# Kernel tuning notes

Hardware: AMD Instinct MI355X
Metric: run time of the kernel (lower is better)

Reference implementation:

```python
import jax, jax.numpy as jnp
import numpy as np

B, S, DDENSE, D, V, F, K = 8192, 26, 13, 32, 100000, 8, 7


def setup_inputs() -> dict:
    key = jax.random.key(0)
    ks = jax.random.split(key, 24)
    n = lambda i, shape, s=0.05: (jax.random.normal(ks[i], shape, dtype=jnp.float32) * s)
    return {
        'sparse_inputs': jax.random.randint(ks[0], (B, S), 0, V),
        'dense_inputs': jax.random.normal(ks[1], (B, DDENSE), dtype=jnp.float32),
        'gen_table': n(2, (V, D), 0.1), 'gen_W': n(3, (DDENSE, D)), 'gen_b': jnp.zeros((D,), jnp.float32),
        'cls_table': n(4, (V, D), 0.1), 'cls_W': n(5, (DDENSE, D)), 'cls_b': jnp.zeros((D,), jnp.float32),
        'conv_k0': n(6, (K, 1, 1, F)), 'conv_b0': jnp.zeros((F,), jnp.float32),
        'fc_W0': n(7, (13 * D * F, 3 * D)), 'fc_b0': jnp.zeros((3 * D,), jnp.float32),
        'conv_k1': n(8, (K, 1, F, F)), 'conv_b1': jnp.zeros((F,), jnp.float32),
        'fc_W1': n(9, (6 * D * F, 3 * D)), 'fc_b1': jnp.zeros((3 * D,), jnp.float32),
        'mlp_W1': n(10, (1584, 128)), 'mlp_b1': jnp.zeros((128,), jnp.float32),
        'bn_gamma': jnp.ones((128,), jnp.float32), 'bn_beta': jnp.zeros((128,), jnp.float32),
        'bn_mean': jnp.zeros((128,), jnp.float32), 'bn_var': jnp.ones((128,), jnp.float32),
        'out_W': n(11, (128, 1)), 'out_b': jnp.zeros((1,), jnp.float32),
    }


def _embed(sparse_inputs, dense_inputs, table, W, b):
    sp = table[sparse_inputs]                       # [B, 26, 32]
    dn = (dense_inputs @ W + b)[:, None, :]         # [B, 1, 32]
    return jnp.concatenate([sp, dn], axis=1)        # [B, 27, 32]


def _conv_tanh(x, k, b):
    y = jax.lax.conv_general_dilated(x, k, (1, 1), 'SAME',
                                     dimension_numbers=('NHWC', 'HWIO', 'NHWC'))
    return jnp.tanh(y + b)


def _maxpool2(x):  # MaxPooling2D((2,1), padding='valid') on NHWC
    return jax.lax.reduce_window(x, -jnp.inf, jax.lax.max,
                                 (1, 2, 1, 1), (1, 2, 1, 1), 'VALID')


def _forward(sparse_inputs, dense_inputs, gen_table, gen_W, gen_b,
             cls_table, cls_W, cls_b, conv_k0, conv_b0, fc_W0, fc_b0,
             conv_k1, conv_b1, fc_W1, fc_b1, mlp_W1, mlp_b1,
             bn_gamma, bn_beta, bn_mean, bn_var, out_W, out_b):
    embs_gen = _embed(sparse_inputs, dense_inputs, gen_table, gen_W, gen_b)
    embs_cls = _embed(sparse_inputs, dense_inputs, cls_table, cls_W, cls_b)

    x = embs_gen[..., None]                         # [B, 27, 32, 1] NHWC
    new_feats = []
    for ck, cb, fw, fb in ((conv_k0, conv_b0, fc_W0, fc_b0),
                           (conv_k1, conv_b1, fc_W1, fc_b1)):
        x = _maxpool2(_conv_tanh(x, ck, cb))
        flat = x.reshape(x.shape[0], -1)
        new_feats.append(jnp.tanh(flat @ fw + fb))  # [B, 96]

    gen = jnp.concatenate(new_feats, axis=1).reshape(x.shape[0], -1, D)  # [B, 6, 32]
    aug = jnp.concatenate([embs_cls, gen], axis=1)                       # [B, 33, 32]

    # pairwise inner products = upper triangle of Gram matrix, combinations order
    gram = jnp.einsum('bnd,bmd->bnm', aug, aug)
    iu, ju = jnp.triu_indices(aug.shape[1], k=1)
    ip = gram[:, iu, ju]                            # [B, 528]

    h = jnp.concatenate([ip, aug.reshape(aug.shape[0], -1)], axis=1)     # [B, 1584]
    h = jax.nn.relu(h @ mlp_W1 + mlp_b1)
    h = (h - bn_mean) * jax.lax.rsqrt(bn_var + 1e-3) * bn_gamma + bn_beta
    return jax.nn.sigmoid(h @ out_W + out_b)        # [B, 1]


def reference(sparse_inputs, dense_inputs, gen_table, gen_W, gen_b,
              cls_table, cls_W, cls_b, conv_k0, conv_b0, fc_W0, fc_b0,
              conv_k1, conv_b1, fc_W1, fc_b1, mlp_W1, mlp_b1,
              bn_gamma, bn_beta, bn_mean, bn_var, out_W, out_b):
    return _forward(sparse_inputs, dense_inputs, gen_table, gen_W, gen_b,
                    cls_table, cls_W, cls_b, conv_k0, conv_b0, fc_W0, fc_b0,
                    conv_k1, conv_b1, fc_W1, fc_b1, mlp_W1, mlp_b1,
                    bn_gamma, bn_beta, bn_mean, bn_var, out_W, out_b)
```

## Files before the change

kernel.cpp:

```cpp
#include <hip/hip_runtime.h>
#include <hip/hip_bf16.h>
#include <math.h>

#define BATCH 8192

typedef _Float16 f16_t;
typedef __attribute__((ext_vector_type(2))) _Float16 h2_t;
typedef __attribute__((ext_vector_type(8))) _Float16 half8;
typedef __attribute__((ext_vector_type(4))) float f32x4;

union U32H2 { unsigned int u; h2_t h; };

__device__ __forceinline__ float fast_tanh(float x) {
    float ax = fabsf(x);
    float e = __expf(ax + ax);
    float t = 1.0f - 2.0f * __builtin_amdgcn_rcpf(e + 1.0f);
    return copysignf(t, x);
}

__device__ __forceinline__ void wpack_one(
    const float* __restrict__ src, f16_t* __restrict__ dst,
    int P, int N, int NT, int Ksrc)
{
    int e = P & 7, lane = (P >> 3) & 63, idx = P >> 9;
    int nt = idx % NT, git = idx / NT;
    int n = nt * 16 + (lane & 15);
    int k = git * 32 + (lane >> 4) * 8 + e;
    dst[P] = (k < Ksrc) ? (f16_t)src[(size_t)k * N + n] : (f16_t)0.f;
}

__global__ __launch_bounds__(256) void k_wpack(
    const float* __restrict__ W0, const float* __restrict__ W1, const float* __restrict__ W2,
    f16_t* __restrict__ Wt0, f16_t* __restrict__ Wt1, f16_t* __restrict__ Wt2)
{
    const int m = blockIdx.y;
    const int P = blockIdx.x * 256 + threadIdx.x;
    if (m == 0)      { if (P < 319488) wpack_one(W0, Wt0, P, 96, 6, 3328); }
    else if (m == 1) { if (P < 147456) wpack_one(W1, Wt1, P, 96, 6, 1536); }
    else             { if (P < 204800) wpack_one(W2, Wt2, P, 128, 8, 1584); }
}

__global__ __launch_bounds__(256, 4) void k_conv_fused(
    const int* __restrict__ sp, const float* __restrict__ dn,
    const float* __restrict__ gen_table, const float* __restrict__ gen_W, const float* __restrict__ gen_b,
    const float* __restrict__ k0, const float* __restrict__ b0,
    const float* __restrict__ k1, const float* __restrict__ b1,
    f16_t* __restrict__ pooled0, f16_t* __restrict__ pooled1)
{
    __shared__ float embGt[2][32][28];
    __shared__ unsigned int x0[2 * 1664];
    __shared__ float k0s[56], k1s[448], b0s[8], b1s[8];
    __shared__ int ids[52];
    __shared__ float dloc[26];
    const int t = threadIdx.x;
    const int half = t >> 7, tt = t & 127;
    const int b = blockIdx.x * 2 + half;

    if (tt < 26) ids[half * 26 + tt] = sp[b * 26 + tt];
    if (tt >= 32 && tt < 45) dloc[half * 13 + tt - 32] = dn[b * 13 + (tt - 32)];
    if (t < 56) k0s[t] = k0[t];
    if (t >= 64 && t < 72) b0s[t - 64] = b0[t - 64];
    if (t >= 72 && t < 80) b1s[t - 72] = b1[t - 72];
    for (int i = t; i < 448; i += 256) k1s[i] = k1[i];
    __syncthreads();

    for (int i = tt; i < 208; i += 128) {
        int s_ = i >> 3, d = (i & 7) * 4;
        float4 v = *(const float4*)(gen_table + (size_t)ids[half * 26 + s_] * 32 + d);
        embGt[half][d][s_] = v.x;
        embGt[half][d + 1][s_] = v.y;
        embGt[half][d + 2][s_] = v.z;
        embGt[half][d + 3][s_] = v.w;
    }
    if (tt < 32) {
        float a = gen_b[tt];
        #pragma unroll
        for (int k = 0; k < 13; k++) a += dloc[half * 13 + k] * gen_W[k * 32 + tt];
        embGt[half][tt][26] = a;
    }
    __syncthreads();

    {
        const int w = tt >> 2, f0 = (tt & 3) * 2;
        const float* xp = &embGt[half][w][0];
        float xr[28];
        #pragma unroll
        for (int q = 0; q < 7; q++) {
            float4 v = *(const float4*)(xp + 4 * q);
            xr[4 * q] = v.x; xr[4 * q + 1] = v.y; xr[4 * q + 2] = v.z; xr[4 * q + 3] = v.w;
        }
        float k0r[7][2];
        #pragma unroll
        for (int tap = 0; tap < 7; tap++) {
            k0r[tap][0] = k0s[tap * 8 + f0];
            k0r[tap][1] = k0s[tap * 8 + f0 + 1];
        }
        const float b00 = b0s[f0], b01 = b0s[f0 + 1];
        unsigned int xloc[13];
        #pragma unroll
        for (int hp = 0; hp < 13; hp++) {
            float p00 = b00, p01 = b01, p10 = b00, p11 = b01;
            #pragma unroll
            for (int tap = 0; tap < 7; tap++) {
                const int h0 = 2 * hp + tap - 3;
                if (h0 >= 0 && h0 < 27) {
                    p00 += xr[h0] * k0r[tap][0];
                    p01 += xr[h0] * k0r[tap][1];
                }
                const int h1 = 2 * hp + 1 + tap - 3;
                if (h1 >= 0 && h1 < 27) {
                    p10 += xr[h1] * k0r[tap][0];
                    p11 += xr[h1] * k0r[tap][1];
                }
            }
            float m0 = fast_tanh(fmaxf(p00, p10));
            float m1 = fast_tanh(fmaxf(p01, p11));
            U32H2 hx; hx.h = h2_t{(f16_t)m0, (f16_t)m1};
            xloc[hp] = hx.u;
        }
        #pragma unroll
        for (int hp = 0; hp < 13; hp++)
            x0[half * 1664 + hp * 128 + tt] = xloc[hp];
    }
    __syncthreads();

    #pragma unroll
    for (int i = t; i < 832; i += 256) {
        int s = (i >= 416) ? 1 : 0;
        int c = i - s * 416;
        int bb = blockIdx.x * 2 + s;
        uint4 v = *(const uint4*)&x0[s * 1664 + c * 4];
        *(uint4*)(pooled0 + (((size_t)(bb >> 4) * 416 + c) * 128 + (bb & 15) * 8)) = v;
    }

    const int w1 = t >> 3, fo = t & 7;
    float m1out[2][6];
    {
        h2_t kh[7][4];
        #pragma unroll
        for (int tap = 0; tap < 7; tap++)
            #pragma unroll
            for (int q = 0; q < 4; q++)
                kh[tap][q] = h2_t{(f16_t)k1s[tap * 64 + (2 * q) * 8 + fo],
                                  (f16_t)k1s[tap * 64 + (2 * q + 1) * 8 + fo]};
        const f16_t bbh = (f16_t)b1s[fo];

        #pragma unroll
        for (int s = 0; s < 2; s++) {
            h2_t acc[12];
            #pragma unroll
            for (int r = 0; r < 12; r++) acc[r] = h2_t{bbh, (f16_t)0.f};
            #pragma unroll
            for (int hh = 0; hh < 13; hh++) {
                uint4 v = *(const uint4*)&x0[s * 1664 + hh * 128 + w1 * 4];
                U32H2 c0, c1, c2, c3;
                c0.u = v.x; c1.u = v.y; c2.u = v.z; c3.u = v.w;
                h2_t x2[4] = { c0.h, c1.h, c2.h, c3.h };
                #pragma unroll
                for (int tap = 0; tap < 7; tap++) {
                    const int r = hh + 3 - tap;
                    if (r >= 0 && r < 12) {
                        #pragma unroll
                        for (int q = 0; q < 4; q++) acc[r] += x2[q] * kh[tap][q];
                    }
                }
            }
            #pragma unroll
            for (int hp = 0; hp < 6; hp++) {
                float a0 = (float)acc[2 * hp][0] + (float)acc[2 * hp][1];
                float a1 = (float)acc[2 * hp + 1][0] + (float)acc[2 * hp + 1][1];
                m1out[s][hp] = fast_tanh(fmaxf(a0, a1));
            }
        }
    }
    __syncthreads();
    f16_t* stg = (f16_t*)&embGt[0][0][0];
    #pragma unroll
    for (int s = 0; s < 2; s++)
        #pragma unroll
        for (int hp = 0; hp < 6; hp++)
            stg[(s * 192 + hp * 32 + w1) * 8 + fo] = (f16_t)m1out[s][hp];
    __syncthreads();
    #pragma unroll
    for (int i = t; i < 384; i += 256) {
        int s = (i >= 192) ? 1 : 0;
        int c = i - s * 192;
        int bs = blockIdx.x * 2 + s;
        uint4 v = *(const uint4*)&stg[(s * 192 + c) * 8];
        *(uint4*)(pooled1 + (((size_t)(bs >> 4) * 192 + c) * 128 + (bs & 15) * 8)) = v;
    }
}

__global__ __launch_bounds__(256) void k_fc_mfma(
    const f16_t* __restrict__ A0, const f16_t* __restrict__ Wt0, float* __restrict__ P0,
    const f16_t* __restrict__ A1, const f16_t* __restrict__ Wt1, float* __restrict__ P1)
{
    const int which = blockIdx.z;
    const f16_t* A  = which ? A1 : A0;
    const f16_t* Wt = which ? Wt1 : Wt0;
    float* P = (which ? P1 : P0) + (size_t)blockIdx.y * (BATCH * 96);
    const int K = which ? 1536 : 3328;
    const int iters = which ? 12 : 26;

    const int t = threadIdx.x, w = t >> 6, l = t & 63;
    const int lane15 = l & 15, quad = l >> 4;
    const int rb = blockIdx.x * 4 + w;
    const int kb = blockIdx.y * (K >> 2);

    const f16_t* ap = A + ((size_t)rb * (K >> 3) + (kb >> 3) + quad) * 128 + lane15 * 8;
    const f16_t* bp = Wt + (size_t)(kb >> 5) * 3072 + l * 8;
    f32x4 acc[6] = {};

    #pragma unroll 2
    for (int it = 0; it < iters; it++) {
        half8 a = *(const half8*)(ap + it * 512);
        #pragma unroll
        for (int nt = 0; nt < 6; nt++) {
            half8 bf = *(const half8*)(bp + it * 3072 + nt * 512);
            acc[nt] = __builtin_amdgcn_mfma_f32_16x16x32_f16(a, bf, acc[nt], 0, 0, 0);
        }
    }
    const int baser = blockIdx.x * 64 + w * 16 + quad * 4;
    #pragma unroll
    for (int nt = 0; nt < 6; nt++)
        #pragma unroll
        for (int i = 0; i < 4; i++)
            P[(size_t)(baser + i) * 96 + nt * 16 + lane15] = acc[nt][i];
}

__global__ __launch_bounds__(256) void k_build_h(
    const int* __restrict__ sp, const float* __restrict__ dn,
    const float* __restrict__ cls_table, const float* __restrict__ cls_W, const float* __restrict__ cls_b,
    const float* __restrict__ p0, const float* __restrict__ fb0,
    const float* __restrict__ p1, const float* __restrict__ fb1,
    f16_t* __restrict__ h)
{
    __shared__ f16_t augs[4][33][40];
    __shared__ float grams[4][32][34];
    __shared__ f16_t hrows[4][1600];
    const int t = threadIdx.x, wv = t >> 6, l = t & 63;
    const int b = blockIdx.x * 4 + wv;
    f16_t (*aug)[40] = augs[wv];
    float (*gram)[34] = grams[wv];
    f16_t* hrow = hrows[wv];

    const int myid = (l < 26) ? sp[b * 26 + l] : 0;

    for (int i = l; i < 416; i += 64) {
        int s_ = i >> 4, d = (i & 15) * 2;
        int id = __shfl(myid, s_);
        float2 v = *(const float2*)(cls_table + (size_t)id * 32 + d);
        U32H2 hx; hx.h = h2_t{(f16_t)v.x, (f16_t)v.y};
        *(unsigned int*)&aug[s_][d] = hx.u;
    }
    if (l < 32) {
        float a = cls_b[l];
        #pragma unroll
        for (int k = 0; k < 13; k++) a += dn[b * 13 + k] * cls_W[k * 32 + l];
        aug[26][l] = (f16_t)a;
    }
    for (int i = l; i < 192; i += 64) {
        int n = 27 + (i >> 5), d = i & 31;
        float s;
        if (i < 96) {
            size_t o = (size_t)b * 96 + i;
            s = p0[o] + p0[o + 786432] + p0[o + 2 * 786432] + p0[o + 3 * 786432] + fb0[i];
        } else {
            int j = i - 96; size_t o = (size_t)b * 96 + j;
            s = p1[o] + p1[o + 786432] + p1[o + 2 * 786432] + p1[o + 3 * 786432] + fb1[j];
        }
        aug[n][d] = (f16_t)fast_tanh(s);
    }

    const int m16 = l & 15, quad = l >> 4;
    half8 a0 = *(const half8*)&aug[m16][quad * 8];
    half8 a1 = *(const half8*)&aug[16 + m16][quad * 8];
    f32x4 c00 = {}, c01 = {}, c11 = {};
    c00 = __builtin_amdgcn_mfma_f32_16x16x32_f16(a0, a0, c00, 0, 0, 0);
    c01 = __builtin_amdgcn_mfma_f32_16x16x32_f16(a0, a1, c01, 0, 0, 0);
    c11 = __builtin_amdgcn_mfma_f32_16x16x32_f16(a1, a1, c11, 0, 0, 0);
    #pragma unroll
    for (int i = 0; i < 4; i++) {
        gram[quad * 4 + i][m16] = c00[i];
        gram[quad * 4 + i][16 + m16] = c01[i];
        gram[16 + quad * 4 + i][16 + m16] = c11[i];
    }
    if (l < 32) {
        float s = 0.f;
        #pragma unroll
        for (int kk = 0; kk < 16; kk++) {
            U32H2 x, y;
            x.u = *(const unsigned int*)&aug[l][2 * kk];
            y.u = *(const unsigned int*)&aug[32][2 * kk];
            s += (float)x.h[0] * (float)y.h[0];
            s += (float)x.h[1] * (float)y.h[1];
        }
        gram[l][32] = s;
    }

    for (int idx = l; idx < 528; idx += 64)
        *(unsigned int*)&hrow[528 + 2 * idx] = *(const unsigned int*)&aug[idx >> 4][(idx & 15) * 2];
    if (l < 8) *(unsigned int*)&hrow[1584 + 2 * l] = 0u;
    for (int pp = l; pp < 264; pp += 64) {
        int p = 2 * pp;
        int i = (int)((65.0f - sqrtf(4225.0f - 8.0f * (float)p)) * 0.5f);
        int st = (i * (65 - i)) >> 1;
        if (st > p) { i--; st = (i * (65 - i)) >> 1; }
        else { int st2 = ((i + 1) * (64 - i)) >> 1; if (st2 <= p) { i++; st = st2; } }
        int j = i + 1 + (p - st);
        float s0, s1;
        if (j < 32) { s0 = gram[i][j]; s1 = gram[i][j + 1]; }
        else        { s0 = gram[i][32]; s1 = gram[i + 1][i + 2]; }
        U32H2 hx; hx.h = h2_t{(f16_t)s0, (f16_t)s1};
        *(unsigned int*)&hrow[p] = hx.u;
    }
    f16_t* hbp = h + ((size_t)(b >> 4) * 200) * 128 + (b & 15) * 8;
    for (int c = l; c < 200; c += 64) {
        uint4 v = *(const uint4*)&hrow[c * 8];
        *(uint4*)(hbp + (size_t)c * 128) = v;
    }
}

__global__ __launch_bounds__(256) void k_mlp_mfma(
    const f16_t* __restrict__ h, const f16_t* __restrict__ Wt2,
    const float* __restrict__ b1, const float* __restrict__ gamma,
    const float* __restrict__ beta, const float* __restrict__ mean,
    const float* __restrict__ var, const float* __restrict__ outW,
    const float* __restrict__ outb, float* __restrict__ out)
{
    __shared__ float lds[2 * 16 * 65];
    __shared__ float red2[32];
    const int t = threadIdx.x, w = t >> 6, l = t & 63;
    const int lane15 = l & 15, quad = l >> 4;
    const int nhalf = w & 1, khalf = w >> 1;

    const f16_t* ap = h + ((size_t)blockIdx.x * 200 + khalf * 100 + quad) * 128 + lane15 * 8;
    const f16_t* bp = Wt2 + ((size_t)khalf * 25 * 8 + nhalf * 4) * 512 + l * 8;
    f32x4 acc[4] = {};

    #pragma unroll 2
    for (int it = 0; it < 25; it++) {
        half8 a = *(const half8*)(ap + it * 512);
        #pragma unroll
        for (int nt = 0; nt < 4; nt++) {
            half8 bf = *(const half8*)(bp + it * 4096 + nt * 512);
            acc[nt] = __builtin_amdgcn_mfma_f32_16x16x32_f16(a, bf, acc[nt], 0, 0, 0);
        }
    }

    if (khalf == 1) {
        #pragma unroll
        for (int nt = 0; nt < 4; nt++)
            #pragma unroll
            for (int i = 0; i < 4; i++)
                lds[nhalf * 1040 + (quad * 4 + i) * 65 + nt * 16 + lane15] = acc[nt][i];
    }
    __syncthreads();
    if (khalf == 0) {
        float pl[4] = { 0.f, 0.f, 0.f, 0.f };
        #pragma unroll
        for (int nt = 0; nt < 4; nt++) {
            int c = nhalf * 64 + nt * 16 + lane15;
            float sc = gamma[c] * rsqrtf(var[c] + 1e-3f);
            float sh = beta[c] - mean[c] * sc;
            float ow = outW[c], bb = b1[c];
            #pragma unroll
            for (int i = 0; i < 4; i++) {
                float v = acc[nt][i] + lds[nhalf * 1040 + (quad * 4 + i) * 65 + nt * 16 + lane15] + bb;
                v = fmaxf(v, 0.f);
                pl[i] += (v * sc + sh) * ow;
            }
        }
        #pragma unroll
        for (int m = 1; m < 16; m <<= 1)
            #pragma unroll
            for (int i = 0; i < 4; i++) pl[i] += __shfl_xor(pl[i], m);
        if (lane15 == 0) {
            #pragma unroll
            for (int i = 0; i < 4; i++) red2[(quad * 4 + i) * 2 + nhalf] = pl[i];
        }
    }
    __syncthreads();
    if (t < 16) {
        float s = red2[t * 2] + red2[t * 2 + 1] + outb[0];
        out[blockIdx.x * 16 + t] = 1.f / (1.f + __expf(-s));
    }
}

extern "C" void kernel_launch(void* const* d_in, const int* in_sizes, int n_in,
                              void* d_out, int out_size, void* d_ws, size_t ws_size,
                              hipStream_t stream) {
    const int*   sp       = (const int*)d_in[0];
    const float* dn       = (const float*)d_in[1];
    const float* gen_tab  = (const float*)d_in[2];
    const float* gen_W    = (const float*)d_in[3];
    const float* gen_b    = (const float*)d_in[4];
    const float* cls_tab  = (const float*)d_in[5];
    const float* cls_W    = (const float*)d_in[6];
    const float* cls_b    = (const float*)d_in[7];
    const float* conv_k0  = (const float*)d_in[8];
    const float* conv_b0  = (const float*)d_in[9];
    const float* fc_W0    = (const float*)d_in[10];
    const float* fc_b0    = (const float*)d_in[11];
    const float* conv_k1  = (const float*)d_in[12];
    const float* conv_b1  = (const float*)d_in[13];
    const float* fc_W1    = (const float*)d_in[14];
    const float* fc_b1    = (const float*)d_in[15];
    const float* mlp_W1   = (const float*)d_in[16];
    const float* mlp_b1   = (const float*)d_in[17];
    const float* bn_gamma = (const float*)d_in[18];
    const float* bn_beta  = (const float*)d_in[19];
    const float* bn_mean  = (const float*)d_in[20];
    const float* bn_var   = (const float*)d_in[21];
    const float* out_W    = (const float*)d_in[22];
    const float* out_b    = (const float*)d_in[23];
    float* out = (float*)d_out;

    char* ws = (char*)d_ws;
    f16_t* pooled0 = (f16_t*)(ws + 0);
    f16_t* pooled1 = (f16_t*)(ws + 54525952ULL);
    float* p0      = (float*)(ws + 79691776ULL);
    float* p1      = (float*)(ws + 92274688ULL);
    f16_t* Wt0     = (f16_t*)(ws + 104857600ULL);
    f16_t* Wt1     = (f16_t*)(ws + 105496576ULL);
    f16_t* Wt2     = (f16_t*)(ws + 105791488ULL);
    f16_t* h       = (f16_t*)(ws + 0);

    k_wpack<<<dim3(1248, 3), 256, 0, stream>>>(fc_W0, fc_W1, mlp_W1, Wt0, Wt1, Wt2);
    k_conv_fused<<<BATCH / 2, 256, 0, stream>>>(sp, dn, gen_tab, gen_W, gen_b,
                                                conv_k0, conv_b0, conv_k1, conv_b1,
                                                pooled0, pooled1);
    k_fc_mfma<<<dim3(BATCH / 64, 4, 2), 256, 0, stream>>>(pooled0, Wt0, p0, pooled1, Wt1, p1);
    k_build_h<<<BATCH / 4, 256, 0, stream>>>(sp, dn, cls_tab, cls_W, cls_b,
                                             p0, fc_b0, p1, fc_b1, h);
    k_mlp_mfma<<<BATCH / 16, 256, 0, stream>>>(h, Wt2, mlp_b1, bn_gamma, bn_beta,
                                               bn_mean, bn_var, out_W, out_b, out);
}
```

Baseline: 250.9 us.

## Drop split-K in FC GEMM and fuse bias+tanh epilogue with f16 output

The FC GEMMs no longer split K into four fp32 partial buffers. Each block now accumulates the full K, adds the bias, applies tanh, and writes f16 features through a shared-memory staging tile. k_build_h then reads those features directly. This removes the partial-sum write/read traffic and one reduction pass, but the grid shrinks to a quarter of the blocks, which lowers occupancy and latency hiding in the FC loop.

```diff
diff --git a/kernel.cpp b/kernel.cpp
--- a/kernel.cpp
+++ b/kernel.cpp
@@ -191,24 +191,27 @@
     }
 }
 
-__global__ __launch_bounds__(256) void k_fc_mfma(
-    const f16_t* __restrict__ A0, const f16_t* __restrict__ Wt0, float* __restrict__ P0,
-    const f16_t* __restrict__ A1, const f16_t* __restrict__ Wt1, float* __restrict__ P1)
-{
-    const int which = blockIdx.z;
+__global__ __launch_bounds__(256) void k_fc(
+    const f16_t* __restrict__ A0, const f16_t* __restrict__ Wt0,
+    const float* __restrict__ fb0, f16_t* __restrict__ F0,
+    const f16_t* __restrict__ A1, const f16_t* __restrict__ Wt1,
+    const float* __restrict__ fb1, f16_t* __restrict__ F1)
+{
+    __shared__ f16_t outstage[64][104];
+    const int which = blockIdx.y;
     const f16_t* A  = which ? A1 : A0;
     const f16_t* Wt = which ? Wt1 : Wt0;
-    float* P = (which ? P1 : P0) + (size_t)blockIdx.y * (BATCH * 96);
+    const float* fb = which ? fb1 : fb0;
+    f16_t* F = which ? F1 : F0;
     const int K = which ? 1536 : 3328;
-    const int iters = which ? 12 : 26;
+    const int iters = which ? 48 : 104;
 
     const int t = threadIdx.x, w = t >> 6, l = t & 63;
     const int lane15 = l & 15, quad = l >> 4;
     const int rb = blockIdx.x * 4 + w;
-    const int kb = blockIdx.y * (K >> 2);
-
-    const f16_t* ap = A + ((size_t)rb * (K >> 3) + (kb >> 3) + quad) * 128 + lane15 * 8;
-    const f16_t* bp = Wt + (size_t)(kb >> 5) * 3072 + l * 8;
+
+    const f16_t* ap = A + ((size_t)rb * (K >> 3) + quad) * 128 + lane15 * 8;
+    const f16_t* bp = Wt + l * 8;
     f32x4 acc[6] = {};
 
     #pragma unroll 2
@@ -220,19 +223,28 @@
             acc[nt] = __builtin_amdgcn_mfma_f32_16x16x32_f16(a, bf, acc[nt], 0, 0, 0);
         }
     }
-    const int baser = blockIdx.x * 64 + w * 16 + quad * 4;
-    #pragma unroll
-    for (int nt = 0; nt < 6; nt++)
+
+    #pragma unroll
+    for (int nt = 0; nt < 6; nt++) {
+        int col = nt * 16 + lane15;
+        float bb = fb[col];
         #pragma unroll
         for (int i = 0; i < 4; i++)
-            P[(size_t)(baser + i) * 96 + nt * 16 + lane15] = acc[nt][i];
+            outstage[w * 16 + quad * 4 + i][col] = (f16_t)fast_tanh(acc[nt][i] + bb);
+    }
+    __syncthreads();
+    #pragma unroll
+    for (int i = t; i < 768; i += 256) {
+        int row = i / 12, c8 = (i % 12) * 8;
+        uint4 v = *(const uint4*)&outstage[row][c8];
+        *(uint4*)(F + ((size_t)blockIdx.x * 64 + row) * 96 + c8) = v;
+    }
 }
 
 __global__ __launch_bounds__(256) void k_build_h(
     const int* __restrict__ sp, const float* __restrict__ dn,
     const float* __restrict__ cls_table, const float* __restrict__ cls_W, const float* __restrict__ cls_b,
-    const float* __restrict__ p0, const float* __restrict__ fb0,
-    const float* __restrict__ p1, const float* __restrict__ fb1,
+    const f16_t* __restrict__ feat0, const f16_t* __restrict__ feat1,
     f16_t* __restrict__ h)
 {
     __shared__ f16_t augs[4][33][40];
@@ -261,15 +273,8 @@
     }
     for (int i = l; i < 192; i += 64) {
         int n = 27 + (i >> 5), d = i & 31;
-        float s;
-        if (i < 96) {
-            size_t o = (size_t)b * 96 + i;
-            s = p0[o] + p0[o + 786432] + p0[o + 2 * 786432] + p0[o + 3 * 786432] + fb0[i];
-        } else {
-            int j = i - 96; size_t o = (size_t)b * 96 + j;
-            s = p1[o] + p1[o + 786432] + p1[o + 2 * 786432] + p1[o + 3 * 786432] + fb1[j];
-        }
-        aug[n][d] = (f16_t)fast_tanh(s);
+        f16_t v = (i < 96) ? feat0[(size_t)b * 96 + i] : feat1[(size_t)b * 96 + (i - 96)];
+        aug[n][d] = v;
     }
 
     const int m16 = l & 15, quad = l >> 4;
@@ -419,20 +424,21 @@
     char* ws = (char*)d_ws;
     f16_t* pooled0 = (f16_t*)(ws + 0);
     f16_t* pooled1 = (f16_t*)(ws + 54525952ULL);
-    float* p0      = (float*)(ws + 79691776ULL);
-    float* p1      = (float*)(ws + 92274688ULL);
-    f16_t* Wt0     = (f16_t*)(ws + 104857600ULL);
-    f16_t* Wt1     = (f16_t*)(ws + 105496576ULL);
-    f16_t* Wt2     = (f16_t*)(ws + 105791488ULL);
+    f16_t* feat0   = (f16_t*)(ws + 79691776ULL);
+    f16_t* feat1   = (f16_t*)(ws + 81264640ULL);
+    f16_t* Wt0     = (f16_t*)(ws + 82837504ULL);
+    f16_t* Wt1     = (f16_t*)(ws + 83476480ULL);
+    f16_t* Wt2     = (f16_t*)(ws + 83771392ULL);
     f16_t* h       = (f16_t*)(ws + 0);
 
     k_wpack<<<dim3(1248, 3), 256, 0, stream>>>(fc_W0, fc_W1, mlp_W1, Wt0, Wt1, Wt2);
     k_conv_fused<<<BATCH / 2, 256, 0, stream>>>(sp, dn, gen_tab, gen_W, gen_b,
                                                 conv_k0, conv_b0, conv_k1, conv_b1,
                                                 pooled0, pooled1);
-    k_fc_mfma<<<dim3(BATCH / 64, 4, 2), 256, 0, stream>>>(pooled0, Wt0, p0, pooled1, Wt1, p1);
+    k_fc<<<dim3(BATCH / 64, 2), 256, 0, stream>>>(pooled0, Wt0, fc_b0, feat0,
+                                                  pooled1, Wt1, fc_b1, feat1);
     k_build_h<<<BATCH / 4, 256, 0, stream>>>(sp, dn, cls_tab, cls_W, cls_b,
-                                             p0, fc_b0, p1, fc_b1, h);
+                                             feat0, feat1, h);
     k_mlp_mfma<<<BATCH / 16, 256, 0, stream>>>(h, Wt2, mlp_b1, bn_gamma, bn_beta,
                                                bn_mean, bn_var, out_W, out_b, out);
 }
```

Measured after the change: 286.6 us. +14.2%, slower.
